# Kernel optimization log

Hardware: AMD Instinct MI355X
Metric: run time of the kernel (lower is better)

The kernel has to match this reference:

```python
import jax, jax.numpy as jnp
import numpy as np

B, F, P, DM = 1, 16, 256, 1024            # batch, frames, patches, mm_hidden_size
HID = 4096                                 # config.hidden_size
DI, DSTATE, DTRANK, DCONV = 2 * DM, 16, DM // 16, 4


def _layernorm(x, w, b):
    mu = x.mean(-1, keepdims=True)
    var = ((x - mu) ** 2).mean(-1, keepdims=True)
    return (x - mu) * jax.lax.rsqrt(var + 1e-5) * w + b


def _selective_scan(u, dt, A, Bm, Cm, Dv):
    # u, dt: [b,L,d]; Bm, Cm: [b,L,n]; A: [d,n]; Dv: [d]
    def step(h, inp):
        dt_t, B_t, C_t, u_t = inp  # [b,d],[b,n],[b,n],[b,d]
        h = jnp.exp(dt_t[..., None] * A) * h + (dt_t * u_t)[..., None] * B_t[:, None, :]
        return h, jnp.einsum('bdn,bn->bd', h, C_t)
    h0 = jnp.zeros((u.shape[0], A.shape[0], A.shape[1]), u.dtype)
    _, ys = jax.lax.scan(step, h0, (jnp.swapaxes(dt, 0, 1), jnp.swapaxes(Bm, 0, 1),
                                    jnp.swapaxes(Cm, 0, 1), jnp.swapaxes(u, 0, 1)))
    return jnp.swapaxes(ys, 0, 1) + u * Dv


def _mamba_block(x, ln_w, ln_b, in_proj_w, conv_w, conv_b, x_proj_w,
                 dt_proj_w, dt_proj_b, A_log, D_param, out_proj_w):
    res = x
    x = _layernorm(x, ln_w, ln_b)
    xz = x @ in_proj_w                       # [b,L,2*DI]
    xin, z = jnp.split(xz, 2, axis=-1)
    xt = jnp.swapaxes(xin, 1, 2)             # [b,DI,L]
    xt = jax.lax.conv_general_dilated(xt, conv_w[:, None, :], (1,), [(DCONV - 1, 0)],
                                      dimension_numbers=('NCH', 'OIH', 'NCH'),
                                      feature_group_count=DI)
    xt = xt + conv_b[:, None]
    u = jax.nn.silu(jnp.swapaxes(xt, 1, 2))  # [b,L,DI]
    x_dbl = u @ x_proj_w                     # [b,L,DTRANK+2*DSTATE]
    dt_raw, Bm, Cm = jnp.split(x_dbl, [DTRANK, DTRANK + DSTATE], axis=-1)
    dt = jax.nn.softplus(dt_raw @ dt_proj_w + dt_proj_b)
    A = -jnp.exp(A_log)
    y = _selective_scan(u, dt, A, Bm, Cm, D_param)
    y = y * jax.nn.silu(z)
    return res + y @ out_proj_w


def setup_inputs() -> dict:
    key = jax.random.key(0)
    ks = jax.random.split(key, 8)
    s = 0.02
    return {
        'vst': jax.random.normal(ks[0], (B, F, P, DM), jnp.float32),
        'ln_w': jnp.ones((DM,), jnp.float32), 'ln_b': jnp.zeros((DM,), jnp.float32),
        'in_proj_w': jax.random.normal(ks[1], (DM, 2 * DI), jnp.float32) * s,
        'conv_w': jax.random.normal(ks[2], (DI, DCONV), jnp.float32) * s,
        'conv_b': jnp.zeros((DI,), jnp.float32),
        'x_proj_w': jax.random.normal(ks[3], (DI, DTRANK + 2 * DSTATE), jnp.float32) * s,
        'dt_proj_w': jax.random.normal(ks[4], (DTRANK, DI), jnp.float32) * s,
        'dt_proj_b': jnp.full((DI,), -4.6, jnp.float32),  # softplus ~ 0.01
        'A_log': jnp.log(jnp.tile(jnp.arange(1, DSTATE + 1, dtype=jnp.float32), (DI, 1))),
        'D_param': jnp.ones((DI,), jnp.float32),
        'out_proj_w': jax.random.normal(ks[5], (DI, DM), jnp.float32) * s,
        'fln_w': jnp.ones((DM,), jnp.float32), 'fln_b': jnp.zeros((DM,), jnp.float32),
        'mlp_w1': jax.random.normal(ks[6], (DM, HID), jnp.float32) * s,
        'mlp_b1': jnp.zeros((HID,), jnp.float32),
        'mlp_w2': jax.random.normal(ks[7], (HID, HID), jnp.float32) * s,
        'mlp_b2': jnp.zeros((HID,), jnp.float32),
    }


def reference(vst, ln_w, ln_b, in_proj_w, conv_w, conv_b, x_proj_w, dt_proj_w,
              dt_proj_b, A_log, D_param, out_proj_w, fln_w, fln_b,
              mlp_w1, mlp_b1, mlp_w2, mlp_b2):
    b, f, p, d = vst.shape
    h = w = int(p ** 0.5)
    # the chain of rearranges in the source is a net reshape to b (f h w) d
    x = vst.reshape(b, f * h * w, d)
    x = _mamba_block(x, ln_w, ln_b, in_proj_w, conv_w, conv_b, x_proj_w,
                     dt_proj_w, dt_proj_b, A_log, D_param, out_proj_w)
    x = _layernorm(x, fln_w, fln_b)
    # AvgPool3d kernel=(1,4,4), stride=(1,4,4) over (f,h,w)
    x = x.reshape(b, f, h // 4, 4, w // 4, 4, d).mean(axis=(3, 5))
    x = x.reshape(b, f * (h // 4) * (w // 4), d)
    y = jax.nn.gelu(x @ mlp_w1 + mlp_b1, approximate=False)
    return y @ mlp_w2 + mlp_b2
```

## Files before the change

kernel.cpp:

```cpp
#include <hip/hip_runtime.h>
#include <hip/hip_bf16.h>
#include <math.h>

typedef __hip_bfloat16 bf16_t;
typedef __attribute__((ext_vector_type(8))) short short8;
typedef __attribute__((ext_vector_type(4))) float f32x4;

#define L_SEQ   4096
#define DMODEL  1024
#define DI      2048
#define NST     16
#define DTRANK  64
#define XDBL_N  96
#define HID     4096
#define CHUNK   32
#define NCHUNK  128
#define POOLED_ROWS 256

__device__ __forceinline__ void async_load16(const bf16_t* g, bf16_t* l) {
    __builtin_amdgcn_global_load_lds(
        (const __attribute__((address_space(1))) void*)g,
        (__attribute__((address_space(3))) void*)l,
        16, 0, 0);
}

__device__ __forceinline__ float bfbits2f(unsigned short b) {
    bf16_t h; *(unsigned short*)&h = b; return __bfloat162float(h);
}

__global__ __launch_bounds__(256)
void transpose_all_kernel(const float* __restrict__ j0, bf16_t* __restrict__ o0,
                          const float* __restrict__ j1, bf16_t* __restrict__ o1,
                          const float* __restrict__ j2, bf16_t* __restrict__ o2,
                          const float* __restrict__ j3, bf16_t* __restrict__ o3,
                          const float* __restrict__ j4, bf16_t* __restrict__ o4,
                          const float* __restrict__ j5, bf16_t* __restrict__ o5) {
    int b = blockIdx.x;
    const float* in; bf16_t* out; int K, N, Npad, local;
    if (b < 1024)       { in = j0; out = o0; K = 1024; N = 4096; Npad = 4096; local = b; }
    else if (b < 1088)  { in = j1; out = o1; K = 2048; N = 96;   Npad = 128;  local = b - 1024; }
    else if (b < 1120)  { in = j2; out = o2; K = 64;   N = 2048; Npad = 2048; local = b - 1088; }
    else if (b < 1632)  { in = j3; out = o3; K = 2048; N = 1024; Npad = 1024; local = b - 1120; }
    else if (b < 2656)  { in = j4; out = o4; K = 1024; N = 4096; Npad = 4096; local = b - 1632; }
    else                { in = j5; out = o5; K = 4096; N = 4096; Npad = 4096; local = b - 2656; }
    int nt = Npad >> 6;
    int k0 = (local / nt) << 6, n0 = (local % nt) << 6;

    __shared__ float t[64 * 65];
    int tid = threadIdx.x;
#pragma unroll
    for (int it = 0; it < 4; it++) {
        int slot = it * 256 + tid;
        int kk = slot >> 4, nq = (slot & 15) * 4;
        int gn = n0 + nq;
        const float* src = in + (size_t)(k0 + kk) * N + gn;
        float4 v;
        if (gn + 3 < N) v = *(const float4*)src;
        else {
            v.x = (gn + 0 < N) ? src[0] : 0.f;
            v.y = (gn + 1 < N) ? src[1] : 0.f;
            v.z = (gn + 2 < N) ? src[2] : 0.f;
            v.w = (gn + 3 < N) ? src[3] : 0.f;
        }
        t[(nq + 0) * 65 + kk] = v.x;
        t[(nq + 1) * 65 + kk] = v.y;
        t[(nq + 2) * 65 + kk] = v.z;
        t[(nq + 3) * 65 + kk] = v.w;
    }
    __syncthreads();
#pragma unroll
    for (int it = 0; it < 2; it++) {
        int slot = it * 256 + tid;
        int nn = slot >> 3, kc = (slot & 7) * 8;
        const float* r = &t[nn * 65 + kc];
        short8 o;
#pragma unroll
        for (int j = 0; j < 8; j++) {
            bf16_t h = __float2bfloat16(r[j]);
            o[j] = *(short*)&h;
        }
        *(short8*)(out + (size_t)(n0 + nn) * K + k0 + kc) = o;
    }
}

__global__ __launch_bounds__(256)
void ln_kernel(const float* __restrict__ x, const float* __restrict__ w,
               const float* __restrict__ b, bf16_t* __restrict__ out) {
    int row = blockIdx.x;
    int tid = threadIdx.x;
    const float* xr = x + (size_t)row * DMODEL;
    float v[4];
    float s = 0.f, ss = 0.f;
#pragma unroll
    for (int e = 0; e < 4; e++) {
        v[e] = xr[tid + e * 256];
        s += v[e];
        ss += v[e] * v[e];
    }
#pragma unroll
    for (int off = 32; off > 0; off >>= 1) {
        s  += __shfl_down(s, off);
        ss += __shfl_down(ss, off);
    }
    __shared__ float rs[4], rss[4];
    int wid = tid >> 6;
    if ((tid & 63) == 0) { rs[wid] = s; rss[wid] = ss; }
    __syncthreads();
    s  = rs[0] + rs[1] + rs[2] + rs[3];
    ss = rss[0] + rss[1] + rss[2] + rss[3];
    float mu  = s * (1.f / DMODEL);
    float var = ss * (1.f / DMODEL) - mu * mu;
    float inv = rsqrtf(var + 1e-5f);
#pragma unroll
    for (int e = 0; e < 4; e++) {
        int col = tid + e * 256;
        out[(size_t)row * DMODEL + col] =
            __float2bfloat16((v[e] - mu) * inv * w[col] + b[col]);
    }
}

__global__ __launch_bounds__(256)
void ln_pool_kernel(const float* __restrict__ x, const float* __restrict__ w,
                    const float* __restrict__ b, bf16_t* __restrict__ pooled) {
    int p = blockIdx.x;
    int tid = threadIdx.x;
    int f = p >> 4, i4 = (p >> 2) & 3, j4 = p & 3;
    __shared__ float rs[4], rss[4];
    float acc[4] = {0.f, 0.f, 0.f, 0.f};
    float wv[4], bv[4];
#pragma unroll
    for (int e = 0; e < 4; e++) { wv[e] = w[tid + e * 256]; bv[e] = b[tid + e * 256]; }
    for (int r16 = 0; r16 < 16; r16++) {
        int ii = r16 >> 2, jj = r16 & 3;
        int row = f * 256 + (i4 * 4 + ii) * 16 + j4 * 4 + jj;
        const float* xr = x + (size_t)row * DMODEL;
        float v[4];
        float s = 0.f, ss = 0.f;
#pragma unroll
        for (int e = 0; e < 4; e++) {
            v[e] = xr[tid + e * 256];
            s += v[e];
            ss += v[e] * v[e];
        }
#pragma unroll
        for (int off = 32; off > 0; off >>= 1) {
            s  += __shfl_down(s, off);
            ss += __shfl_down(ss, off);
        }
        int wid = tid >> 6;
        if ((tid & 63) == 0) { rs[wid] = s; rss[wid] = ss; }
        __syncthreads();
        s  = rs[0] + rs[1] + rs[2] + rs[3];
        ss = rss[0] + rss[1] + rss[2] + rss[3];
        float mu  = s * (1.f / DMODEL);
        float var = ss * (1.f / DMODEL) - mu * mu;
        float inv = rsqrtf(var + 1e-5f);
#pragma unroll
        for (int e = 0; e < 4; e++)
            acc[e] += (v[e] - mu) * inv * wv[e] + bv[e];
        __syncthreads();
    }
#pragma unroll
    for (int e = 0; e < 4; e++)
        pooled[(size_t)p * DMODEL + tid + e * 256] = __float2bfloat16(acc[e] * (1.f / 16.f));
}

template <int EPI>
__global__ __launch_bounds__(256, 2)
void mfma_gemm(const bf16_t* __restrict__ A, int lda,
               const bf16_t* __restrict__ Bt, int ldb,
               int K,
               float* __restrict__ Cf, bf16_t* __restrict__ Cb, int ldc,
               const float* __restrict__ bias, const float* __restrict__ res) {
    __shared__ bf16_t Asl[128 * 32];
    __shared__ bf16_t Bsl[128 * 32];
    const int tid = threadIdx.x;
    const int l = tid & 63, w = tid >> 6;
    const int m0 = blockIdx.y * 128, n0 = blockIdx.x * 128;
    const int wm = (w >> 1) * 64, wn = (w & 1) * 64;

    const int srow = tid >> 2;
    const int skc = (tid & 3) * 8;
    const bf16_t* Ag = A + (size_t)(m0 + srow) * lda + skc;
    const bf16_t* Bg = Bt + (size_t)(n0 + srow) * ldb + skc;
    bf16_t* As0 = Asl + (size_t)(w * 64) * 8;
    bf16_t* As1 = Asl + (size_t)(256 + w * 64) * 8;
    bf16_t* Bs0 = Bsl + (size_t)(w * 64) * 8;
    bf16_t* Bs1 = Bsl + (size_t)(256 + w * 64) * 8;

    f32x4 acc[4][4];
#pragma unroll
    for (int i = 0; i < 4; i++)
#pragma unroll
        for (int j = 0; j < 4; j++) acc[i][j] = (f32x4){0.f, 0.f, 0.f, 0.f};

    const short8* Asv = (const short8*)Asl;
    const short8* Bsv = (const short8*)Bsl;
    const int fr = l >> 4;
    const int fc = l & 15;

    for (int k0 = 0; k0 < K; k0 += 32) {
        __syncthreads();
        async_load16(Ag, As0);
        async_load16(Ag + (size_t)64 * lda, As1);
        async_load16(Bg, Bs0);
        async_load16(Bg + (size_t)64 * ldb, Bs1);
        Ag += 32; Bg += 32;
        __syncthreads();

        short8 a[4], b[4];
#pragma unroll
        for (int im = 0; im < 4; im++)
            a[im] = Asv[(wm + im * 16 + fc) * 4 + fr];
#pragma unroll
        for (int in = 0; in < 4; in++)
            b[in] = Bsv[(wn + in * 16 + fc) * 4 + fr];
#pragma unroll
        for (int im = 0; im < 4; im++)
#pragma unroll
            for (int in = 0; in < 4; in++)
                acc[im][in] = __builtin_amdgcn_mfma_f32_16x16x32_bf16(
                    a[im], b[in], acc[im][in], 0, 0, 0);
    }

#pragma unroll
    for (int im = 0; im < 4; im++) {
        int mbase = m0 + wm + im * 16 + fr * 4;
#pragma unroll
        for (int in = 0; in < 4; in++) {
            int n = n0 + wn + in * 16 + fc;
            float bv = (EPI == 1) ? bias[n] : 0.f;
#pragma unroll
            for (int v = 0; v < 4; v++) {
                float x = acc[im][in][v];
                size_t off = (size_t)(mbase + v) * ldc + n;
                if (EPI == 0) {
                    Cb[off] = __float2bfloat16(x);
                } else if (EPI == 1) {
                    x += bv;
                    x = (x > 20.f) ? x : log1pf(__expf(x));
                    Cb[off] = __float2bfloat16(x);
                }
            }
        }
    }
}

template <bool PBF16>
__global__ __launch_bounds__(256, 2)
void mfma_gemm_splitk(const bf16_t* __restrict__ A, int lda,
                      const bf16_t* __restrict__ Bt, int ldb,
                      int Kper, void* __restrict__ Cpart, int ldc,
                      size_t pstride) {
    __shared__ bf16_t Asl[128 * 32];
    __shared__ bf16_t Bsl[128 * 32];
    const int tid = threadIdx.x;
    const int l = tid & 63, w = tid >> 6;
    const int m0 = blockIdx.y * 128, n0 = blockIdx.x * 128;
    const int wm = (w >> 1) * 64, wn = (w & 1) * 64;
    const int kbase = blockIdx.z * Kper;

    const int srow = tid >> 2;
    const int skc = (tid & 3) * 8;
    const bf16_t* Ag = A + (size_t)(m0 + srow) * lda + kbase + skc;
    const bf16_t* Bg = Bt + (size_t)(n0 + srow) * ldb + kbase + skc;
    bf16_t* As0 = Asl + (size_t)(w * 64) * 8;
    bf16_t* As1 = Asl + (size_t)(256 + w * 64) * 8;
    bf16_t* Bs0 = Bsl + (size_t)(w * 64) * 8;
    bf16_t* Bs1 = Bsl + (size_t)(256 + w * 64) * 8;

    f32x4 acc[4][4];
#pragma unroll
    for (int i = 0; i < 4; i++)
#pragma unroll
        for (int j = 0; j < 4; j++) acc[i][j] = (f32x4){0.f, 0.f, 0.f, 0.f};

    const short8* Asv = (const short8*)Asl;
    const short8* Bsv = (const short8*)Bsl;
    const int fr = l >> 4;
    const int fc = l & 15;

    for (int k0 = 0; k0 < Kper; k0 += 32) {
        __syncthreads();
        async_load16(Ag, As0);
        async_load16(Ag + (size_t)64 * lda, As1);
        async_load16(Bg, Bs0);
        async_load16(Bg + (size_t)64 * ldb, Bs1);
        Ag += 32; Bg += 32;
        __syncthreads();

        short8 a[4], b[4];
#pragma unroll
        for (int im = 0; im < 4; im++)
            a[im] = Asv[(wm + im * 16 + fc) * 4 + fr];
#pragma unroll
        for (int in = 0; in < 4; in++)
            b[in] = Bsv[(wn + in * 16 + fc) * 4 + fr];
#pragma unroll
        for (int im = 0; im < 4; im++)
#pragma unroll
            for (int in = 0; in < 4; in++)
                acc[im][in] = __builtin_amdgcn_mfma_f32_16x16x32_bf16(
                    a[im], b[in], acc[im][in], 0, 0, 0);
    }

#pragma unroll
    for (int im = 0; im < 4; im++) {
        int mbase = m0 + wm + im * 16 + fr * 4;
#pragma unroll
        for (int in = 0; in < 4; in++) {
            int n = n0 + wn + in * 16 + fc;
#pragma unroll
            for (int v = 0; v < 4; v++) {
                size_t o = (size_t)(mbase + v) * ldc + n;
                if (PBF16)
                    ((bf16_t*)Cpart)[(size_t)blockIdx.z * pstride + o] =
                        __float2bfloat16(acc[im][in][v]);
                else
                    ((float*)Cpart)[(size_t)blockIdx.z * pstride + o] = acc[im][in][v];
            }
        }
    }
}

template <int S, int EPI>
__global__ __launch_bounds__(256)
void reduce_splitk(const float* __restrict__ part, size_t pstride, int ldp,
                   int M, int N, float* __restrict__ outf, bf16_t* __restrict__ outb,
                   int ldo, const float* __restrict__ bias) {
    int idx = blockIdx.x * 256 + threadIdx.x;
    if (idx >= M * N) return;
    int r = idx / N, c = idx - r * N;
    float s = 0.f;
#pragma unroll
    for (int z = 0; z < S; z++)
        s += part[(size_t)z * pstride + (size_t)r * ldp + c];
    size_t o = (size_t)r * ldo + c;
    if (EPI == 0) {
        outf[o] = s;
        outb[o] = __float2bfloat16(s);
    } else if (EPI == 1) {
        s += bias[c];
        s = 0.5f * s * (1.f + erff(s * 0.70710678118654752f));
        outb[o] = __float2bfloat16(s);
    } else {
        outf[o] = s + bias[c];
    }
}

__global__ __launch_bounds__(256)
void reduce2_res_kernel(const bf16_t* __restrict__ part, size_t pstride,
                        const float* __restrict__ res, float* __restrict__ outf,
                        int total4) {
    int idx = blockIdx.x * 256 + threadIdx.x;
    if (idx >= total4) return;
    size_t o = (size_t)idx * 4;
    ushort4 p0 = *(const ushort4*)((const unsigned short*)part + o);
    ushort4 p1 = *(const ushort4*)((const unsigned short*)part + pstride + o);
    float4 r = *(const float4*)(res + o);
    float4 ov;
    ov.x = bfbits2f(p0.x) + bfbits2f(p1.x) + r.x;
    ov.y = bfbits2f(p0.y) + bfbits2f(p1.y) + r.y;
    ov.z = bfbits2f(p0.z) + bfbits2f(p1.z) + r.z;
    ov.w = bfbits2f(p0.w) + bfbits2f(p1.w) + r.w;
    *(float4*)(outf + o) = ov;
}

__global__ __launch_bounds__(256)
void conv_silu_kernel(const bf16_t* __restrict__ xz, const float* __restrict__ cw,
                      const float* __restrict__ cb, bf16_t* __restrict__ u) {
    int idx = blockIdx.x * 256 + threadIdx.x;
    if (idx >= L_SEQ * DI) return;
    int ch = idx & (DI - 1);
    int l  = idx >> 11;
    float acc = cb[ch];
#pragma unroll
    for (int k = 0; k < 4; k++) {
        int ls = l - 3 + k;
        if (ls >= 0)
            acc += cw[ch * 4 + k] * __bfloat162float(xz[(size_t)ls * (2 * DI) + ch]);
    }
    u[idx] = __float2bfloat16(acc / (1.f + __expf(-acc)));
}

__global__ __launch_bounds__(256)
void scan_pass1(const bf16_t* __restrict__ dt, const bf16_t* __restrict__ u,
                const float* __restrict__ x_dbl, const float* __restrict__ A_log,
                float* __restrict__ Pw, float* __restrict__ Sw) {
    int c = blockIdx.x;
    int tid = threadIdx.x;
    int lane = tid & 63, w = tid >> 6;
    int dloc = w * 32 + (lane & 31);
    int n0 = (lane >> 5) * 8;
    int d = blockIdx.y * 128 + dloc;
    int l0 = c * CHUNK;
    __shared__ float sB[CHUNK * NST];
    for (int i = tid; i < CHUNK * NST; i += 256)
        sB[i] = x_dbl[(size_t)(l0 + (i >> 4)) * XDBL_N + DTRANK + (i & 15)];
    __syncthreads();
    float Areg[8], h[8];
#pragma unroll
    for (int j = 0; j < 8; j++) {
        Areg[j] = -__expf(A_log[d * NST + n0 + j]);
        h[j] = 0.f;
    }
    float dts = 0.f;
    float dtl = __bfloat162float(dt[(size_t)l0 * DI + d]);
    float ul  = __bfloat162float(u[(size_t)l0 * DI + d]);
    for (int l = 0; l < CHUNK; l++) {
        float dtn = 0.f, un = 0.f;
        if (l + 1 < CHUNK) {
            int gl = l0 + l + 1;
            dtn = __bfloat162float(dt[(size_t)gl * DI + d]);
            un  = __bfloat162float(u[(size_t)gl * DI + d]);
        }
        float du = dtl * ul;
        dts += dtl;
#pragma unroll
        for (int j = 0; j < 8; j++) {
            float a = __expf(dtl * Areg[j]);
            h[j] = a * h[j] + du * sB[l * NST + n0 + j];
        }
        dtl = dtn; ul = un;
    }
    size_t base = ((size_t)c * DI + d) * NST + n0;
#pragma unroll
    for (int j = 0; j < 8; j++) {
        Pw[base + j] = __expf(dts * Areg[j]);
        Sw[base + j] = h[j];
    }
}

__global__ __launch_bounds__(256)
void scan_pass2(const float* __restrict__ Pw, float* __restrict__ SwInit) {
    int tid = blockIdx.x * 256 + threadIdx.x;
    if (tid >= DI * NST) return;
    float h = 0.f;
    for (int c = 0; c < NCHUNK; c++) {
        size_t idx = (size_t)c * (DI * NST) + tid;
        float s = SwInit[idx];
        SwInit[idx] = h;
        h = Pw[idx] * h + s;
    }
}

__global__ __launch_bounds__(256)
void scan_pass3(const bf16_t* __restrict__ dt, const bf16_t* __restrict__ u,
                const float* __restrict__ x_dbl, const float* __restrict__ A_log,
                const float* __restrict__ Dp, const float* __restrict__ initw,
                const bf16_t* __restrict__ xz, bf16_t* __restrict__ yy) {
    int c = blockIdx.x;
    int tid = threadIdx.x;
    int lane = tid & 63, w = tid >> 6;
    int dloc = w * 32 + (lane & 31);
    int n0 = (lane >> 5) * 8;
    int d = blockIdx.y * 128 + dloc;
    int l0 = c * CHUNK;
    __shared__ float sBC[CHUNK * 2 * NST];
    for (int i = tid; i < CHUNK * 2 * NST; i += 256)
        sBC[i] = x_dbl[(size_t)(l0 + (i >> 5)) * XDBL_N + DTRANK + (i & 31)];
    __syncthreads();
    float Areg[8], h[8];
    size_t base = ((size_t)c * DI + d) * NST + n0;
#pragma unroll
    for (int j = 0; j < 8; j++) {
        Areg[j] = -__expf(A_log[d * NST + n0 + j]);
        h[j] = initw[base + j];
    }
    float Dd = Dp[d];
    float dtl = __bfloat162float(dt[(size_t)l0 * DI + d]);
    float ul  = __bfloat162float(u[(size_t)l0 * DI + d]);
    float zv  = __bfloat162float(xz[(size_t)l0 * (2 * DI) + DI + d]);
    for (int l = 0; l < CHUNK; l++) {
        float dtn = 0.f, un = 0.f, zn = 0.f;
        if (l + 1 < CHUNK) {
            int gl = l0 + l + 1;
            dtn = __bfloat162float(dt[(size_t)gl * DI + d]);
            un  = __bfloat162float(u[(size_t)gl * DI + d]);
            zn  = __bfloat162float(xz[(size_t)gl * (2 * DI) + DI + d]);
        }
        float du = dtl * ul;
        float y = 0.f;
#pragma unroll
        for (int j = 0; j < 8; j++) {
            float a = __expf(dtl * Areg[j]);
            h[j] = a * h[j] + du * sBC[l * 32 + n0 + j];
            y += h[j] * sBC[l * 32 + NST + n0 + j];
        }
        y += __shfl_xor(y, 32);
        float sz = zv / (1.f + __expf(-zv));
        if ((lane >> 5) == 0)
            yy[(size_t)(l0 + l) * DI + d] = __float2bfloat16((y + ul * Dd) * sz);
        dtl = dtn; ul = un; zv = zn;
    }
}

extern "C" void kernel_launch(void* const* d_in, const int* in_sizes, int n_in,
                              void* d_out, int out_size, void* d_ws, size_t ws_size,
                              hipStream_t stream) {
    const float* vst        = (const float*)d_in[0];
    const float* ln_w       = (const float*)d_in[1];
    const float* ln_b       = (const float*)d_in[2];
    const float* in_proj_w  = (const float*)d_in[3];
    const float* conv_w     = (const float*)d_in[4];
    const float* conv_b     = (const float*)d_in[5];
    const float* x_proj_w   = (const float*)d_in[6];
    const float* dt_proj_w  = (const float*)d_in[7];
    const float* dt_proj_b  = (const float*)d_in[8];
    const float* A_log      = (const float*)d_in[9];
    const float* D_param    = (const float*)d_in[10];
    const float* out_proj_w = (const float*)d_in[11];
    const float* fln_w      = (const float*)d_in[12];
    const float* fln_b      = (const float*)d_in[13];
    const float* mlp_w1     = (const float*)d_in[14];
    const float* mlp_b1     = (const float*)d_in[15];
    const float* mlp_w2     = (const float*)d_in[16];
    const float* mlp_b2     = (const float*)d_in[17];
    float* out = (float*)d_out;

    char* wsb = (char*)d_ws;
    size_t off = 0;
    auto alloc_bf = [&](size_t n) { bf16_t* p = (bf16_t*)(wsb + off); off += n * 2; return p; };
    auto alloc_f  = [&](size_t n) { float*  p = (float*)(wsb + off); off += n * 4; return p; };

    bf16_t* w1t  = alloc_bf((size_t)(2 * DI) * DMODEL);
    bf16_t* xpt  = alloc_bf((size_t)128 * DI);
    bf16_t* dtpt = alloc_bf((size_t)DI * DTRANK);
    bf16_t* opt  = alloc_bf((size_t)DMODEL * DI);
    bf16_t* m1t  = alloc_bf((size_t)HID * DMODEL);
    bf16_t* m2t  = alloc_bf((size_t)HID * HID);
    bf16_t* xz_bf   = alloc_bf((size_t)L_SEQ * 2 * DI);
    bf16_t* u_bf    = alloc_bf((size_t)L_SEQ * DI);
    bf16_t* dt_bf   = alloc_bf((size_t)L_SEQ * DI);
    bf16_t* xdbl_bf = alloc_bf((size_t)L_SEQ * XDBL_N);
    bf16_t* yy_bf   = alloc_bf((size_t)L_SEQ * DI);
    float*  xdbl_f  = alloc_f((size_t)L_SEQ * XDBL_N);
    float*  Pw      = alloc_f((size_t)NCHUNK * DI * NST);
    float*  Sw      = alloc_f((size_t)NCHUNK * DI * NST);
    bf16_t* xn_bf   = yy_bf;
    float*  g2part  = Pw;
    float*  x2_f    = Pw;
    bf16_t* g4part  = xz_bf;
    bf16_t* pooled  = dt_bf;
    bf16_t* h1_bf   = dt_bf + (size_t)POOLED_ROWS * DMODEL;
    float*  g5part  = (float*)yy_bf;
    float*  g6part  = (float*)xz_bf;

    dim3 blk256(256);

    transpose_all_kernel<<<6752, blk256, 0, stream>>>(
        in_proj_w, w1t, x_proj_w, xpt, dt_proj_w, dtpt,
        out_proj_w, opt, mlp_w1, m1t, mlp_w2, m2t);

    ln_kernel<<<L_SEQ, blk256, 0, stream>>>(vst, ln_w, ln_b, xn_bf);

    mfma_gemm<0><<<dim3((2 * DI) / 128, L_SEQ / 128), blk256, 0, stream>>>(
        xn_bf, DMODEL, w1t, DMODEL, DMODEL, nullptr, xz_bf, 2 * DI, nullptr, nullptr);

    conv_silu_kernel<<<(L_SEQ * DI) / 256, blk256, 0, stream>>>(xz_bf, conv_w, conv_b, u_bf);

    mfma_gemm_splitk<false><<<dim3(1, L_SEQ / 128, 8), blk256, 0, stream>>>(
        u_bf, DI, xpt, DI, DI / 8, g2part, 128, (size_t)L_SEQ * 128);
    reduce_splitk<8, 0><<<(L_SEQ * XDBL_N) / 256, blk256, 0, stream>>>(
        g2part, (size_t)L_SEQ * 128, 128, L_SEQ, XDBL_N, xdbl_f, xdbl_bf, XDBL_N, nullptr);

    mfma_gemm<1><<<dim3(DI / 128, L_SEQ / 128), blk256, 0, stream>>>(
        xdbl_bf, XDBL_N, dtpt, DTRANK, DTRANK, nullptr, dt_bf, DI, dt_proj_b, nullptr);

    scan_pass1<<<dim3(NCHUNK, DI / 128), blk256, 0, stream>>>(
        dt_bf, u_bf, xdbl_f, A_log, Pw, Sw);
    scan_pass2<<<(DI * NST) / 256, blk256, 0, stream>>>(Pw, Sw);
    scan_pass3<<<dim3(NCHUNK, DI / 128), blk256, 0, stream>>>(
        dt_bf, u_bf, xdbl_f, A_log, D_param, Sw, xz_bf, yy_bf);

    mfma_gemm_splitk<true><<<dim3(DMODEL / 128, L_SEQ / 128, 2), blk256, 0, stream>>>(
        yy_bf, DI, opt, DI, DI / 2, g4part, DMODEL, (size_t)L_SEQ * DMODEL);
    reduce2_res_kernel<<<(L_SEQ * DMODEL / 4) / 256, blk256, 0, stream>>>(
        g4part, (size_t)L_SEQ * DMODEL, vst, x2_f, L_SEQ * DMODEL / 4);

    ln_pool_kernel<<<POOLED_ROWS, blk256, 0, stream>>>(x2_f, fln_w, fln_b, pooled);

    mfma_gemm_splitk<false><<<dim3(HID / 128, POOLED_ROWS / 128, 4), blk256, 0, stream>>>(
        pooled, DMODEL, m1t, DMODEL, DMODEL / 4, g5part, HID, (size_t)POOLED_ROWS * HID);
    reduce_splitk<4, 1><<<(POOLED_ROWS * HID) / 256, blk256, 0, stream>>>(
        g5part, (size_t)POOLED_ROWS * HID, HID, POOLED_ROWS, HID, nullptr, h1_bf, HID, mlp_b1);

    mfma_gemm_splitk<false><<<dim3(HID / 128, POOLED_ROWS / 128, 8), blk256, 0, stream>>>(
        h1_bf, HID, m2t, HID, HID / 8, g6part, HID, (size_t)POOLED_ROWS * HID);
    reduce_splitk<8, 2><<<(POOLED_ROWS * HID) / 256, blk256, 0, stream>>>(
        g6part, (size_t)POOLED_ROWS * HID, HID, POOLED_ROWS, HID, out, nullptr, HID, mlp_b2);
}
```

Measured before the change: 493.1 us.

## Fuse residual split-K reduce into LN-pool, widen transpose tiles, prefetch scan pass2

The separate reduce2_res kernel is removed. Its residual add of the two bf16 split-K partials is folded into the final layernorm+avgpool kernel, so the fp32 x2 intermediate is never written or re-read. The weight transpose kernel now processes 128x64 tiles, halving the block count, with a K bound guard for the small K=64 matrix. scan_pass2 software-prefetches the next chunk's P/S values to hide the latency of its serial loop. The pool kernel now does scalar bf16 loads of the partials instead of vectorized ones, and the transpose uses more LDS per block.

```diff
diff --git a/kernel.cpp b/kernel.cpp
--- a/kernel.cpp
+++ b/kernel.cpp
@@ -37,42 +37,46 @@
                           const float* __restrict__ j5, bf16_t* __restrict__ o5) {
     int b = blockIdx.x;
     const float* in; bf16_t* out; int K, N, Npad, local;
-    if (b < 1024)       { in = j0; out = o0; K = 1024; N = 4096; Npad = 4096; local = b; }
-    else if (b < 1088)  { in = j1; out = o1; K = 2048; N = 96;   Npad = 128;  local = b - 1024; }
-    else if (b < 1120)  { in = j2; out = o2; K = 64;   N = 2048; Npad = 2048; local = b - 1088; }
-    else if (b < 1632)  { in = j3; out = o3; K = 2048; N = 1024; Npad = 1024; local = b - 1120; }
-    else if (b < 2656)  { in = j4; out = o4; K = 1024; N = 4096; Npad = 4096; local = b - 1632; }
-    else                { in = j5; out = o5; K = 4096; N = 4096; Npad = 4096; local = b - 2656; }
+    if (b < 512)        { in = j0; out = o0; K = 1024; N = 4096; Npad = 4096; local = b; }
+    else if (b < 544)   { in = j1; out = o1; K = 2048; N = 96;   Npad = 128;  local = b - 512; }
+    else if (b < 576)   { in = j2; out = o2; K = 64;   N = 2048; Npad = 2048; local = b - 544; }
+    else if (b < 832)   { in = j3; out = o3; K = 2048; N = 1024; Npad = 1024; local = b - 576; }
+    else if (b < 1344)  { in = j4; out = o4; K = 1024; N = 4096; Npad = 4096; local = b - 832; }
+    else                { in = j5; out = o5; K = 4096; N = 4096; Npad = 4096; local = b - 1344; }
     int nt = Npad >> 6;
-    int k0 = (local / nt) << 6, n0 = (local % nt) << 6;
-
-    __shared__ float t[64 * 65];
+    int k0 = (local / nt) << 7, n0 = (local % nt) << 6;
+
+    __shared__ float t[64 * 129];
     int tid = threadIdx.x;
+    int kkb = tid >> 4;
+    int nq  = (tid & 15) * 4;
+#pragma unroll
+    for (int it = 0; it < 8; it++) {
+        int kl = it * 16 + kkb;
+        int gk = k0 + kl, gn = n0 + nq;
+        float4 v = {0.f, 0.f, 0.f, 0.f};
+        if (gk < K) {
+            const float* src = in + (size_t)gk * N + gn;
+            if (gn + 3 < N) v = *(const float4*)src;
+            else {
+                if (gn + 0 < N) v.x = src[0];
+                if (gn + 1 < N) v.y = src[1];
+                if (gn + 2 < N) v.z = src[2];
+                if (gn + 3 < N) v.w = src[3];
+            }
+        }
+        t[(nq + 0) * 129 + kl] = v.x;
+        t[(nq + 1) * 129 + kl] = v.y;
+        t[(nq + 2) * 129 + kl] = v.z;
+        t[(nq + 3) * 129 + kl] = v.w;
+    }
+    __syncthreads();
 #pragma unroll
     for (int it = 0; it < 4; it++) {
         int slot = it * 256 + tid;
-        int kk = slot >> 4, nq = (slot & 15) * 4;
-        int gn = n0 + nq;
-        const float* src = in + (size_t)(k0 + kk) * N + gn;
-        float4 v;
-        if (gn + 3 < N) v = *(const float4*)src;
-        else {
-            v.x = (gn + 0 < N) ? src[0] : 0.f;
-            v.y = (gn + 1 < N) ? src[1] : 0.f;
-            v.z = (gn + 2 < N) ? src[2] : 0.f;
-            v.w = (gn + 3 < N) ? src[3] : 0.f;
-        }
-        t[(nq + 0) * 65 + kk] = v.x;
-        t[(nq + 1) * 65 + kk] = v.y;
-        t[(nq + 2) * 65 + kk] = v.z;
-        t[(nq + 3) * 65 + kk] = v.w;
-    }
-    __syncthreads();
-#pragma unroll
-    for (int it = 0; it < 2; it++) {
-        int slot = it * 256 + tid;
-        int nn = slot >> 3, kc = (slot & 7) * 8;
-        const float* r = &t[nn * 65 + kc];
+        int nn = slot >> 4, kc = (slot & 15) * 8;
+        if (k0 + kc >= K) continue;
+        const float* r = &t[nn * 129 + kc];
         short8 o;
 #pragma unroll
         for (int j = 0; j < 8; j++) {
@@ -120,8 +124,9 @@
 }
 
 __global__ __launch_bounds__(256)
-void ln_pool_kernel(const float* __restrict__ x, const float* __restrict__ w,
-                    const float* __restrict__ b, bf16_t* __restrict__ pooled) {
+void ln_pool2_kernel(const bf16_t* __restrict__ part, size_t pstride,
+                     const float* __restrict__ res, const float* __restrict__ w,
+                     const float* __restrict__ b, bf16_t* __restrict__ pooled) {
     int p = blockIdx.x;
     int tid = threadIdx.x;
     int f = p >> 4, i4 = (p >> 2) & 3, j4 = p & 3;
@@ -133,14 +138,18 @@
     for (int r16 = 0; r16 < 16; r16++) {
         int ii = r16 >> 2, jj = r16 & 3;
         int row = f * 256 + (i4 * 4 + ii) * 16 + j4 * 4 + jj;
-        const float* xr = x + (size_t)row * DMODEL;
+        size_t ro = (size_t)row * DMODEL;
         float v[4];
         float s = 0.f, ss = 0.f;
 #pragma unroll
         for (int e = 0; e < 4; e++) {
-            v[e] = xr[tid + e * 256];
-            s += v[e];
-            ss += v[e] * v[e];
+            int col = tid + e * 256;
+            float x = res[ro + col]
+                    + __bfloat162float(part[ro + col])
+                    + __bfloat162float(part[pstride + ro + col]);
+            v[e] = x;
+            s += x;
+            ss += x * x;
         }
 #pragma unroll
         for (int off = 32; off > 0; off >>= 1) {
@@ -346,24 +355,6 @@
     } else {
         outf[o] = s + bias[c];
     }
-}
-
-__global__ __launch_bounds__(256)
-void reduce2_res_kernel(const bf16_t* __restrict__ part, size_t pstride,
-                        const float* __restrict__ res, float* __restrict__ outf,
-                        int total4) {
-    int idx = blockIdx.x * 256 + threadIdx.x;
-    if (idx >= total4) return;
-    size_t o = (size_t)idx * 4;
-    ushort4 p0 = *(const ushort4*)((const unsigned short*)part + o);
-    ushort4 p1 = *(const ushort4*)((const unsigned short*)part + pstride + o);
-    float4 r = *(const float4*)(res + o);
-    float4 ov;
-    ov.x = bfbits2f(p0.x) + bfbits2f(p1.x) + r.x;
-    ov.y = bfbits2f(p0.y) + bfbits2f(p1.y) + r.y;
-    ov.z = bfbits2f(p0.z) + bfbits2f(p1.z) + r.z;
-    ov.w = bfbits2f(p0.w) + bfbits2f(p1.w) + r.w;
-    *(float4*)(outf + o) = ov;
 }
 
 __global__ __launch_bounds__(256)
@@ -435,12 +426,17 @@
 void scan_pass2(const float* __restrict__ Pw, float* __restrict__ SwInit) {
     int tid = blockIdx.x * 256 + threadIdx.x;
     if (tid >= DI * NST) return;
+    const int DN = DI * NST;
+    size_t idx = tid;
     float h = 0.f;
+    float p = Pw[idx], s = SwInit[idx];
     for (int c = 0; c < NCHUNK; c++) {
-        size_t idx = (size_t)c * (DI * NST) + tid;
-        float s = SwInit[idx];
+        size_t nidx = idx + DN;
+        float pn = 0.f, sn = 0.f;
+        if (c + 1 < NCHUNK) { pn = Pw[nidx]; sn = SwInit[nidx]; }
         SwInit[idx] = h;
-        h = Pw[idx] * h + s;
+        h = p * h + s;
+        p = pn; s = sn; idx = nidx;
     }
 }
 
@@ -539,7 +535,6 @@
     float*  Sw      = alloc_f((size_t)NCHUNK * DI * NST);
     bf16_t* xn_bf   = yy_bf;
     float*  g2part  = Pw;
-    float*  x2_f    = Pw;
     bf16_t* g4part  = xz_bf;
     bf16_t* pooled  = dt_bf;
     bf16_t* h1_bf   = dt_bf + (size_t)POOLED_ROWS * DMODEL;
@@ -548,7 +543,7 @@
 
     dim3 blk256(256);
 
-    transpose_all_kernel<<<6752, blk256, 0, stream>>>(
+    transpose_all_kernel<<<3392, blk256, 0, stream>>>(
         in_proj_w, w1t, x_proj_w, xpt, dt_proj_w, dtpt,
         out_proj_w, opt, mlp_w1, m1t, mlp_w2, m2t);
 
@@ -575,10 +570,9 @@
 
     mfma_gemm_splitk<true><<<dim3(DMODEL / 128, L_SEQ / 128, 2), blk256, 0, stream>>>(
         yy_bf, DI, opt, DI, DI / 2, g4part, DMODEL, (size_t)L_SEQ * DMODEL);
-    reduce2_res_kernel<<<(L_SEQ * DMODEL / 4) / 256, blk256, 0, stream>>>(
-        g4part, (size_t)L_SEQ * DMODEL, vst, x2_f, L_SEQ * DMODEL / 4);
-
-    ln_pool_kernel<<<POOLED_ROWS, blk256, 0, stream>>>(x2_f, fln_w, fln_b, pooled);
+
+    ln_pool2_kernel<<<POOLED_ROWS, blk256, 0, stream>>>(
+        g4part, (size_t)L_SEQ * DMODEL, vst, fln_w, fln_b, pooled);
 
     mfma_gemm_splitk<false><<<dim3(HID / 128, POOLED_ROWS / 128, 4), blk256, 0, stream>>>(
         pooled, DMODEL, m1t, DMODEL, DMODEL / 4, g5part, HID, (size_t)POOLED_ROWS * HID);
```

Result: no change. 483.6 us (-1.9%).
